# Optimization experiments

Hardware: AMD Instinct MI355X
Metric: run time of the kernel (lower is better)

## Reference

```python
import jax, jax.numpy as jnp
import numpy as np

DIM = 1024
N = 65536

def _l2norm(x):
    # F.normalize: x / max(||x||_2, eps) along last dim, eps=1e-12
    n = jnp.linalg.norm(x, axis=-1, keepdims=True)
    return x / jnp.maximum(n, 1e-12)

def setup_inputs() -> dict:
    key = jax.random.key(0)
    ks = jax.random.split(key, 10)
    s = 0.02
    return {
        "q_init": jax.random.normal(ks[0], (1, DIM), jnp.float32),
        "k_init": jax.random.normal(ks[1], (N, DIM), jnp.float32),
        "Wq": jax.random.normal(ks[2], (DIM, DIM // 2), jnp.float32) * s,
        "bq": jnp.zeros((DIM // 2,), jnp.float32),
        "Wk": jax.random.normal(ks[3], (DIM, DIM // 2), jnp.float32) * s,
        "bk": jnp.zeros((DIM // 2,), jnp.float32),
        "Wv": jax.random.normal(ks[4], (DIM, DIM), jnp.float32) * s,
        "bv": jnp.zeros((DIM,), jnp.float32),
        "Wm": jax.random.normal(ks[5], (DIM, DIM), jnp.float32) * s,
        "bm": jnp.zeros((DIM,), jnp.float32),
        "gamma": jnp.ones((1,), jnp.float32),
    }

def reference(q_init, k_init, Wq, bq, Wk, bk, Wv, bv, Wm, bm, gamma):
    q = _l2norm(q_init) @ Wq + bq              # [1, dim/2]
    kn = _l2norm(k_init)                        # [N, dim]
    k = kn @ Wk + bk                            # [N, dim/2]
    v = kn @ Wv + bv                            # [N, dim]
    scores = q @ k.T                            # [1, N]
    # global mean/std rescale (torch.std is unbiased, ddof=1)
    scores = (scores - scores.mean()) / (jnp.std(scores, ddof=1) + 1e-8)
    attn = jax.nn.softmax(jnp.clip(scores, -10.0, 10.0), axis=-1)
    # dropout is identity in eval mode
    out = (attn @ v) @ Wm + bm                  # [1, dim]
    g = jax.nn.sigmoid(gamma)                   # [1]
    return g * q_init + (1.0 - g) * out
```

## Files before the change

### kernel.cpp

```cpp
#include <hip/hip_runtime.h>
#include <math.h>

#define DIM   1024
#define HALF  512
#define NROWS 65536
#define SBLK  4096
#define WBLK  2048
#define WF1   64

#define OFF_SCAL   0
#define OFF_QACC   (OFF_SCAL + 8)
#define OFF_PVEC   (OFF_QACC + HALF)
#define OFF_PSTAT  (OFF_PVEC + DIM)
#define OFF_S      (OFF_PSTAT + 2*SBLK)
#define OFF_INVN   (OFF_S + NROWS)
#define OFF_PESUM  (OFF_INVN + NROWS)
#define OFF_PW     (OFF_PESUM + WBLK)
#define OFF_P2     (OFF_PW + WBLK*DIM)
#define OFF_WACC   (OFF_P2 + WF1*DIM)
#define OFF_OVACC  (OFF_WACC + DIM)
#define OFF_END    (OFF_OVACC + DIM)

__global__ void k_prep(const float* __restrict__ q_init,
                       const float* __restrict__ Wq,
                       float* __restrict__ qacc) {
    __shared__ float qs[DIM];
    __shared__ float4 red4[256];
    __shared__ float red[256];
    int t = threadIdx.x, c4 = blockIdx.x;
    float sq = 0.f;
    #pragma unroll
    for (int i = 0; i < 4; ++i) {
        float v = q_init[t + i * 256];
        qs[t + i * 256] = v;
        sq += v * v;
    }
    red[t] = sq;
    __syncthreads();
    for (int s = 128; s > 0; s >>= 1) {
        if (t < s) red[t] += red[t + s];
        __syncthreads();
    }
    float inv = 1.0f / fmaxf(sqrtf(red[0]), 1e-12f);
    const float4* W4 = (const float4*)Wq;
    float4 acc = make_float4(0.f, 0.f, 0.f, 0.f);
    for (int r = t; r < DIM; r += 256) {
        float c = qs[r] * inv;
        float4 m = W4[(size_t)r * (HALF / 4) + c4];
        acc.x += c * m.x; acc.y += c * m.y; acc.z += c * m.z; acc.w += c * m.w;
    }
    red4[t] = acc;
    __syncthreads();
    for (int s = 128; s > 0; s >>= 1) {
        if (t < s) {
            red4[t].x += red4[t + s].x; red4[t].y += red4[t + s].y;
            red4[t].z += red4[t + s].z; red4[t].w += red4[t + s].w;
        }
        __syncthreads();
    }
    if (t == 0) ((float4*)qacc)[c4] = red4[0];
}

__global__ void k_pvec(const float* __restrict__ Wk,
                       const float* __restrict__ qacc,
                       const float* __restrict__ bq,
                       float* __restrict__ pvec) {
    __shared__ float q[HALF];
    int t = threadIdx.x;
    for (int j = t; j < HALF; j += 256) q[j] = qacc[j] + bq[j];
    __syncthreads();
    int wave = t >> 6, lane = t & 63;
    int d = blockIdx.x * 4 + wave;
    const float* row = Wk + (size_t)d * HALF;
    float acc = 0.f;
    #pragma unroll
    for (int j0 = 0; j0 < HALF; j0 += 64) acc += row[j0 + lane] * q[j0 + lane];
    #pragma unroll
    for (int o = 32; o > 0; o >>= 1) acc += __shfl_down(acc, o);
    if (lane == 0) pvec[d] = acc;
}

__global__ void k_scores(const float* __restrict__ K,
                         const float* __restrict__ pvec,
                         float* __restrict__ svals,
                         float* __restrict__ invn,
                         float2* __restrict__ pstat) {
    __shared__ float4 p4s[256];
    __shared__ float wsum[4], wssq[4];
    int t = threadIdx.x;
    p4s[t] = ((const float4*)pvec)[t];
    __syncthreads();
    int wave = t >> 6, lane = t & 63;
    int row0 = blockIdx.x * 16 + wave * 4;
    const float4* k4 = (const float4*)K + (size_t)row0 * 256 + lane;
    float4 v[16];
    #pragma unroll
    for (int r = 0; r < 4; ++r)
        #pragma unroll
        for (int i = 0; i < 4; ++i)
            v[r * 4 + i] = k4[r * 256 + i * 64];
    float d[4] = {0, 0, 0, 0}, q[4] = {0, 0, 0, 0};
    #pragma unroll
    for (int r = 0; r < 4; ++r) {
        #pragma unroll
        for (int i = 0; i < 4; ++i) {
            float4 a = v[r * 4 + i];
            float4 p = p4s[lane + i * 64];
            d[r] += a.x * p.x + a.y * p.y + a.z * p.z + a.w * p.w;
            q[r] += a.x * a.x + a.y * a.y + a.z * a.z + a.w * a.w;
        }
    }
    #pragma unroll
    for (int o = 32; o > 0; o >>= 1) {
        #pragma unroll
        for (int r = 0; r < 4; ++r) {
            d[r] += __shfl_down(d[r], o);
            q[r] += __shfl_down(q[r], o);
        }
    }
    if (lane == 0) {
        float i0 = 1.0f / fmaxf(sqrtf(q[0]), 1e-12f);
        float i1 = 1.0f / fmaxf(sqrtf(q[1]), 1e-12f);
        float i2 = 1.0f / fmaxf(sqrtf(q[2]), 1e-12f);
        float i3 = 1.0f / fmaxf(sqrtf(q[3]), 1e-12f);
        float s0 = d[0] * i0, s1 = d[1] * i1, s2 = d[2] * i2, s3 = d[3] * i3;
        *(float4*)(svals + row0) = make_float4(s0, s1, s2, s3);
        *(float4*)(invn + row0) = make_float4(i0, i1, i2, i3);
        wsum[wave] = s0 + s1 + s2 + s3;
        wssq[wave] = s0 * s0 + s1 * s1 + s2 * s2 + s3 * s3;
    }
    __syncthreads();
    if (t == 0)
        pstat[blockIdx.x] = make_float2(wsum[0] + wsum[1] + wsum[2] + wsum[3],
                                        wssq[0] + wssq[1] + wssq[2] + wssq[3]);
}

__global__ void k_redstats(const float2* __restrict__ pstat, float* __restrict__ scal) {
    __shared__ float rs[1024], rq[1024];
    int t = threadIdx.x;
    float s = 0.f, q = 0.f;
    for (int i = t; i < SBLK; i += 1024) {
        float2 p = pstat[i];
        s += p.x; q += p.y;
    }
    rs[t] = s; rq[t] = q;
    __syncthreads();
    for (int k = 512; k > 0; k >>= 1) {
        if (t < k) { rs[t] += rs[t + k]; rq[t] += rq[t + k]; }
        __syncthreads();
    }
    if (t == 0) {
        float mean = rs[0] / (float)NROWS;
        float var  = (rq[0] - (float)NROWS * mean * mean) / (float)(NROWS - 1);
        scal[0] = mean;
        scal[1] = 1.0f / (sqrtf(fmaxf(var, 0.0f)) + 1e-8f);
    }
}

__global__ void k_wsum(const float* __restrict__ K,
                       const float* __restrict__ svals,
                       const float* __restrict__ invn,
                       const float* __restrict__ scal,
                       float* __restrict__ pw,
                       float* __restrict__ pesum) {
    int t = threadIdx.x;
    int b = (int)gridDim.x - 1 - (int)blockIdx.x;
    int r0 = b * 32;
    float mean = scal[0], rstd = scal[1];
    const float4* M4 = (const float4*)K + (size_t)r0 * 256 + t;
    float4 acc = make_float4(0.f, 0.f, 0.f, 0.f);
    float esum = 0.f;
    #pragma unroll
    for (int rb = 0; rb < 32; rb += 8) {
        float4 m[8];
        #pragma unroll
        for (int r = 0; r < 8; ++r) m[r] = M4[(size_t)(rb + r) * 256];
        #pragma unroll
        for (int r = 0; r < 8; ++r) {
            int ri = r0 + rb + r;
            float z = (svals[ri] - mean) * rstd;
            z = fminf(fmaxf(z, -10.0f), 10.0f);
            float e = expf(z);
            esum += e;
            float c = e * invn[ri];
            acc.x += c * m[r].x; acc.y += c * m[r].y;
            acc.z += c * m[r].z; acc.w += c * m[r].w;
        }
    }
    ((float4*)pw)[(size_t)b * 256 + t] = acc;
    if (t == 0) pesum[b] = esum;
}

__global__ void k_wfold(const float* __restrict__ pw, float* __restrict__ p2) {
    int t = threadIdx.x, b = blockIdx.x;
    const float4* pw4 = (const float4*)pw;
    float4 acc = make_float4(0.f, 0.f, 0.f, 0.f);
    #pragma unroll
    for (int p = 0; p < WBLK / WF1; ++p) {
        float4 m = pw4[(size_t)(b * (WBLK / WF1) + p) * 256 + t];
        acc.x += m.x; acc.y += m.y; acc.z += m.z; acc.w += m.w;
    }
    ((float4*)p2)[b * 256 + t] = acc;
}

__global__ void k_wreduce(const float* __restrict__ p2,
                          const float* __restrict__ pesum,
                          float* __restrict__ wacc) {
    __shared__ float red[1024];
    int t = threadIdx.x;
    float es = 0.f;
    for (int i = t; i < WBLK; i += 1024) es += pesum[i];
    red[t] = es;
    __syncthreads();
    for (int s = 512; s > 0; s >>= 1) {
        if (t < s) red[t] += red[t + s];
        __syncthreads();
    }
    float inv = 1.0f / red[0];
    float acc = 0.f;
    #pragma unroll
    for (int b = 0; b < WF1; ++b) acc += p2[b * DIM + t];
    wacc[t] = acc * inv;
}

__global__ void k_mv(const float* __restrict__ M,
                     const float* __restrict__ coeff,
                     const float* __restrict__ cbias,
                     float* __restrict__ out) {
    __shared__ float4 red[256];
    int t = threadIdx.x, c4 = blockIdx.x;
    const float4* M4 = (const float4*)M;
    float4 acc = make_float4(0.f, 0.f, 0.f, 0.f);
    for (int r = t; r < DIM; r += 256) {
        float c = coeff[r];
        if (cbias) c += cbias[r];
        float4 m = M4[(size_t)r * (DIM / 4) + c4];
        acc.x += c * m.x; acc.y += c * m.y; acc.z += c * m.z; acc.w += c * m.w;
    }
    red[t] = acc;
    __syncthreads();
    for (int s = 128; s > 0; s >>= 1) {
        if (t < s) {
            red[t].x += red[t + s].x; red[t].y += red[t + s].y;
            red[t].z += red[t + s].z; red[t].w += red[t + s].w;
        }
        __syncthreads();
    }
    if (t == 0) ((float4*)out)[c4] = red[0];
}

__global__ void k_mv_final(const float* __restrict__ M,
                           const float* __restrict__ coeff,
                           const float* __restrict__ cbias,
                           const float* __restrict__ q_init,
                           const float* __restrict__ bm,
                           const float* __restrict__ gamma,
                           float* __restrict__ out) {
    __shared__ float4 red[256];
    int t = threadIdx.x, c4 = blockIdx.x;
    const float4* M4 = (const float4*)M;
    float4 acc = make_float4(0.f, 0.f, 0.f, 0.f);
    for (int r = t; r < DIM; r += 256) {
        float c = coeff[r] + cbias[r];
        float4 m = M4[(size_t)r * (DIM / 4) + c4];
        acc.x += c * m.x; acc.y += c * m.y; acc.z += c * m.z; acc.w += c * m.w;
    }
    red[t] = acc;
    __syncthreads();
    for (int s = 128; s > 0; s >>= 1) {
        if (t < s) {
            red[t].x += red[t + s].x; red[t].y += red[t + s].y;
            red[t].z += red[t + s].z; red[t].w += red[t + s].w;
        }
        __syncthreads();
    }
    if (t == 0) {
        float g = 1.0f / (1.0f + expf(-gamma[0]));
        float4 qv = ((const float4*)q_init)[c4];
        float4 bmv = ((const float4*)bm)[c4];
        float4 o;
        o.x = g * qv.x + (1.0f - g) * (red[0].x + bmv.x);
        o.y = g * qv.y + (1.0f - g) * (red[0].y + bmv.y);
        o.z = g * qv.z + (1.0f - g) * (red[0].z + bmv.z);
        o.w = g * qv.w + (1.0f - g) * (red[0].w + bmv.w);
        ((float4*)out)[c4] = o;
    }
}

extern "C" void kernel_launch(void* const* d_in, const int* in_sizes, int n_in,
                              void* d_out, int out_size, void* d_ws, size_t ws_size,
                              hipStream_t stream) {
    const float* q_init = (const float*)d_in[0];
    const float* k_init = (const float*)d_in[1];
    const float* Wq     = (const float*)d_in[2];
    const float* bq     = (const float*)d_in[3];
    const float* Wk     = (const float*)d_in[4];
    const float* Wv     = (const float*)d_in[6];
    const float* bv     = (const float*)d_in[7];
    const float* Wm     = (const float*)d_in[8];
    const float* bm     = (const float*)d_in[9];
    const float* gamma  = (const float*)d_in[10];
    float* out = (float*)d_out;
    float* ws  = (float*)d_ws;

    float*  scal   = ws + OFF_SCAL;
    float*  qacc   = ws + OFF_QACC;
    float*  pvec   = ws + OFF_PVEC;
    float2* pstat  = (float2*)(ws + OFF_PSTAT);
    float*  svals  = ws + OFF_S;
    float*  invn   = ws + OFF_INVN;
    float*  pesum  = ws + OFF_PESUM;
    float*  pw     = ws + OFF_PW;
    float*  p2     = ws + OFF_P2;
    float*  wacc   = ws + OFF_WACC;
    float*  ovacc  = ws + OFF_OVACC;

    k_prep<<<HALF / 4, 256, 0, stream>>>(q_init, Wq, qacc);
    k_pvec<<<DIM / 4, 256, 0, stream>>>(Wk, qacc, bq, pvec);
    k_scores<<<SBLK, 256, 0, stream>>>(k_init, pvec, svals, invn, pstat);
    k_redstats<<<1, 1024, 0, stream>>>(pstat, scal);
    k_wsum<<<WBLK, 256, 0, stream>>>(k_init, svals, invn, scal, pw, pesum);
    k_wfold<<<WF1, 256, 0, stream>>>(pw, p2);
    k_wreduce<<<1, 1024, 0, stream>>>(p2, pesum, wacc);
    k_mv<<<DIM / 4, 256, 0, stream>>>(Wv, wacc, nullptr, ovacc);
    k_mv_final<<<DIM / 4, 256, 0, stream>>>(Wm, ovacc, bv, q_init, bm, gamma, out);
}
```

Baseline: 472.5 us.

## Rework score kernel lane mapping and halve rows per wsum block

```diff
diff --git a/kernel.cpp b/kernel.cpp
--- a/kernel.cpp
+++ b/kernel.cpp
@@ -5,7 +5,7 @@
 #define HALF  512
 #define NROWS 65536
 #define SBLK  4096
-#define WBLK  2048
+#define WBLK  4096
 #define WF1   64
 
 #define OFF_SCAL   0
@@ -16,10 +16,9 @@
 #define OFF_INVN   (OFF_S + NROWS)
 #define OFF_PESUM  (OFF_INVN + NROWS)
 #define OFF_PW     (OFF_PESUM + WBLK)
-#define OFF_P2     (OFF_PW + WBLK*DIM)
+#define OFF_P2     (OFF_PW + (size_t)WBLK*DIM)
 #define OFF_WACC   (OFF_P2 + WF1*DIM)
 #define OFF_OVACC  (OFF_WACC + DIM)
-#define OFF_END    (OFF_OVACC + DIM)
 
 __global__ void k_prep(const float* __restrict__ q_init,
                        const float* __restrict__ Wq,
@@ -44,7 +43,9 @@
     float inv = 1.0f / fmaxf(sqrtf(red[0]), 1e-12f);
     const float4* W4 = (const float4*)Wq;
     float4 acc = make_float4(0.f, 0.f, 0.f, 0.f);
-    for (int r = t; r < DIM; r += 256) {
+    #pragma unroll
+    for (int i = 0; i < 4; ++i) {
+        int r = t + i * 256;
         float c = qs[r] * inv;
         float4 m = W4[(size_t)r * (HALF / 4) + c4];
         acc.x += c * m.x; acc.y += c * m.y; acc.z += c * m.z; acc.w += c * m.w;
@@ -80,59 +81,52 @@
     if (lane == 0) pvec[d] = acc;
 }
 
-__global__ void k_scores(const float* __restrict__ K,
-                         const float* __restrict__ pvec,
-                         float* __restrict__ svals,
-                         float* __restrict__ invn,
-                         float2* __restrict__ pstat) {
-    __shared__ float4 p4s[256];
-    __shared__ float wsum[4], wssq[4];
-    int t = threadIdx.x;
-    p4s[t] = ((const float4*)pvec)[t];
-    __syncthreads();
+__global__ __launch_bounds__(256)
+void k_scores(const float* __restrict__ K,
+              const float* __restrict__ pvec,
+              float* __restrict__ svals,
+              float* __restrict__ invn,
+              float2* __restrict__ pstat) {
+    __shared__ float sb[8];
+    int t = threadIdx.x;
     int wave = t >> 6, lane = t & 63;
-    int row0 = blockIdx.x * 16 + wave * 4;
-    const float4* k4 = (const float4*)K + (size_t)row0 * 256 + lane;
-    float4 v[16];
-    #pragma unroll
-    for (int r = 0; r < 4; ++r)
-        #pragma unroll
-        for (int i = 0; i < 4; ++i)
-            v[r * 4 + i] = k4[r * 256 + i * 64];
-    float d[4] = {0, 0, 0, 0}, q[4] = {0, 0, 0, 0};
-    #pragma unroll
-    for (int r = 0; r < 4; ++r) {
-        #pragma unroll
-        for (int i = 0; i < 4; ++i) {
-            float4 a = v[r * 4 + i];
-            float4 p = p4s[lane + i * 64];
-            d[r] += a.x * p.x + a.y * p.y + a.z * p.z + a.w * p.w;
-            q[r] += a.x * a.x + a.y * a.y + a.z * a.z + a.w * a.w;
-        }
-    }
-    #pragma unroll
-    for (int o = 32; o > 0; o >>= 1) {
-        #pragma unroll
-        for (int r = 0; r < 4; ++r) {
-            d[r] += __shfl_down(d[r], o);
-            q[r] += __shfl_down(q[r], o);
-        }
-    }
-    if (lane == 0) {
-        float i0 = 1.0f / fmaxf(sqrtf(q[0]), 1e-12f);
-        float i1 = 1.0f / fmaxf(sqrtf(q[1]), 1e-12f);
-        float i2 = 1.0f / fmaxf(sqrtf(q[2]), 1e-12f);
-        float i3 = 1.0f / fmaxf(sqrtf(q[3]), 1e-12f);
-        float s0 = d[0] * i0, s1 = d[1] * i1, s2 = d[2] * i2, s3 = d[3] * i3;
-        *(float4*)(svals + row0) = make_float4(s0, s1, s2, s3);
-        *(float4*)(invn + row0) = make_float4(i0, i1, i2, i3);
-        wsum[wave] = s0 + s1 + s2 + s3;
-        wssq[wave] = s0 * s0 + s1 * s1 + s2 * s2 + s3 * s3;
-    }
+    int sub = lane & 15;
+    int row = blockIdx.x * 16 + wave * 4 + (lane >> 4);
+
+    const float4* p4 = (const float4*)pvec;
+    float4 p[16];
+    #pragma unroll
+    for (int i = 0; i < 16; ++i) p[i] = p4[sub + 16 * i];
+
+    const float4* k4 = (const float4*)K + (size_t)row * 256 + sub;
+    float dot = 0.f, sq = 0.f;
+    #pragma unroll
+    for (int i = 0; i < 16; ++i) {
+        float4 a = k4[16 * i];
+        dot += a.x * p[i].x + a.y * p[i].y + a.z * p[i].z + a.w * p[i].w;
+        sq  += a.x * a.x + a.y * a.y + a.z * a.z + a.w * a.w;
+    }
+    #pragma unroll
+    for (int o = 8; o > 0; o >>= 1) {
+        dot += __shfl_down(dot, o);
+        sq  += __shfl_down(sq, o);
+    }
+    float sv = 0.f;
+    if (sub == 0) {
+        float inv = 1.0f / fmaxf(sqrtf(sq), 1e-12f);
+        sv = dot * inv;
+        svals[row] = sv;
+        invn[row]  = inv;
+    }
+    float ss = (sub == 0) ? sv : 0.f;
+    float qq = (sub == 0) ? sv * sv : 0.f;
+    ss += __shfl_down(ss, 16); qq += __shfl_down(qq, 16);
+    ss += __shfl_down(ss, 32); qq += __shfl_down(qq, 32);
+    if (lane == 0) { sb[wave] = ss; sb[4 + wave] = qq; }
     __syncthreads();
     if (t == 0)
-        pstat[blockIdx.x] = make_float2(wsum[0] + wsum[1] + wsum[2] + wsum[3],
-                                        wssq[0] + wssq[1] + wssq[2] + wssq[3]);
+        pstat[blockIdx.x] = make_float2(sb[0] + sb[1] + sb[2] + sb[3],
+                                        sb[4] + sb[5] + sb[6] + sb[7]);
 }
 
 __global__ void k_redstats(const float2* __restrict__ pstat, float* __restrict__ scal) {
@@ -157,26 +151,27 @@
     }
 }
 
-__global__ void k_wsum(const float* __restrict__ K,
-                       const float* __restrict__ svals,
-                       const float* __restrict__ invn,
-                       const float* __restrict__ scal,
-                       float* __restrict__ pw,
-                       float* __restrict__ pesum) {
+__global__ __launch_bounds__(256)
+void k_wsum(const float* __restrict__ K,
+            const float* __restrict__ svals,
+            const float* __restrict__ invn,
+            const float* __restrict__ scal,
+            float* __restrict__ pw,
+            float* __restrict__ pesum) {
     int t = threadIdx.x;
     int b = (int)gridDim.x - 1 - (int)blockIdx.x;
-    int r0 = b * 32;
+    int r0 = b * 16;
     float mean = scal[0], rstd = scal[1];
     const float4* M4 = (const float4*)K + (size_t)r0 * 256 + t;
     float4 acc = make_float4(0.f, 0.f, 0.f, 0.f);
     float esum = 0.f;
     #pragma unroll
-    for (int rb = 0; rb < 32; rb += 8) {
-        float4 m[8];
+    for (int rb = 0; rb < 16; rb += 4) {
+        float4 m[4];
         #pragma unroll
-        for (int r = 0; r < 8; ++r) m[r] = M4[(size_t)(rb + r) * 256];
+        for (int r = 0; r < 4; ++r) m[r] = M4[(size_t)(rb + r) * 256];
         #pragma unroll
-        for (int r = 0; r < 8; ++r) {
+        for (int r = 0; r < 4; ++r) {
             int ri = r0 + rb + r;
             float z = (svals[ri] - mean) * rstd;
             z = fminf(fmaxf(z, -10.0f), 10.0f);
@@ -195,7 +190,6 @@
     int t = threadIdx.x, b = blockIdx.x;
     const float4* pw4 = (const float4*)pw;
     float4 acc = make_float4(0.f, 0.f, 0.f, 0.f);
-    #pragma unroll
     for (int p = 0; p < WBLK / WF1; ++p) {
         float4 m = pw4[(size_t)(b * (WBLK / WF1) + p) * 256 + t];
         acc.x += m.x; acc.y += m.y; acc.z += m.z; acc.w += m.w;
@@ -225,15 +219,15 @@
 
 __global__ void k_mv(const float* __restrict__ M,
                      const float* __restrict__ coeff,
-                     const float* __restrict__ cbias,
                      float* __restrict__ out) {
     __shared__ float4 red[256];
     int t = threadIdx.x, c4 = blockIdx.x;
     const float4* M4 = (const float4*)M;
     float4 acc = make_float4(0.f, 0.f, 0.f, 0.f);
-    for (int r = t; r < DIM; r += 256) {
+    #pragma unroll
+    for (int i = 0; i < 4; ++i) {
+        int r = t + i * 256;
         float c = coeff[r];
-        if (cbias) c += cbias[r];
         float4 m = M4[(size_t)r * (DIM / 4) + c4];
         acc.x += c * m.x; acc.y += c * m.y; acc.z += c * m.z; acc.w += c * m.w;
     }
@@ -260,7 +254,9 @@
     int t = threadIdx.x, c4 = blockIdx.x;
     const float4* M4 = (const float4*)M;
     float4 acc = make_float4(0.f, 0.f, 0.f, 0.f);
-    for (int r = t; r < DIM; r += 256) {
+    #pragma unroll
+    for (int i = 0; i < 4; ++i) {
+        int r = t + i * 256;
         float c = coeff[r] + cbias[r];
         float4 m = M4[(size_t)r * (DIM / 4) + c4];
         acc.x += c * m.x; acc.y += c * m.y; acc.z += c * m.z; acc.w += c * m.w;
@@ -276,14 +272,13 @@
     }
     if (t == 0) {
         float g = 1.0f / (1.0f + expf(-gamma[0]));
-        float4 qv = ((const float4*)q_init)[c4];
+        float4 qv  = ((const float4*)q_init)[c4];
         float4 bmv = ((const float4*)bm)[c4];
-        float4 o;
-        o.x = g * qv.x + (1.0f - g) * (red[0].x + bmv.x);
-        o.y = g * qv.y + (1.0f - g) * (red[0].y + bmv.y);
-        o.z = g * qv.z + (1.0f - g) * (red[0].z + bmv.z);
-        o.w = g * qv.w + (1.0f - g) * (red[0].w + bmv.w);
-        ((float4*)out)[c4] = o;
+        ((float4*)out)[c4] = make_float4(
+            g * qv.x + (1.0f - g) * (red[0].x + bmv.x),
+            g * qv.y + (1.0f - g) * (red[0].y + bmv.y),
+            g * qv.z + (1.0f - g) * (red[0].z + bmv.z),
+            g * qv.w + (1.0f - g) * (red[0].w + bmv.w));
     }
 }
 
@@ -322,6 +317,6 @@
     k_wsum<<<WBLK, 256, 0, stream>>>(k_init, svals, invn, scal, pw, pesum);
     k_wfold<<<WF1, 256, 0, stream>>>(pw, p2);
     k_wreduce<<<1, 1024, 0, stream>>>(p2, pesum, wacc);
-    k_mv<<<DIM / 4, 256, 0, stream>>>(Wv, wacc, nullptr, ovacc);
+    k_mv<<<DIM / 4, 256, 0, stream>>>(Wv, wacc, ovacc);
     k_mv_final<<<DIM / 4, 256, 0, stream>>>(Wm, ovacc, bv, q_init, bm, gamma, out);
 }
```

Result: no change. 479.7 us (+1.5%).
